# Optimization experiments

Hardware: AMD Instinct MI355X
Metric: run time of the kernel (lower is better)

## Reference

```python
import jax, jax.numpy as jnp
import numpy as np

B, H, D = 512, 2048, 4096          # batch, mem_hid_dim, r_dim + r2_dim
MAXITER = 100
LR = 0.01                          # mem_step_size
TOL = 1e-6
B1, B2, EPS = 0.9, 0.999, 1e-8     # torch.optim.Adam defaults


def setup_inputs() -> dict:
    key = jax.random.key(0)
    k = jax.random.split(key, 5)
    x = jax.random.normal(k[0], (B, D), jnp.float32)
    W = jax.random.normal(k[1], (D, H), jnp.float32) * 0.02   # mem.weight (out, in)
    c = jax.random.normal(k[2], (D,), jnp.float32) * 0.01     # mem.bias
    b = jax.random.normal(k[3], (H,), jnp.float32) * 0.01     # prior mean self.b
    r0 = jax.random.normal(k[4], (B, H), jnp.float32) * 0.025 # init_code_
    return {"x": x, "W": W, "c": c, "b": b, "r0": r0}


def _infer(x, W, c, b, r0):
    batch = x.shape[0]

    def loss_and_grad(r):
        diff = x - (r @ W.T + c)                         # (B, D) residual
        pr = r - b                                       # (B, H) prior residual
        loss = (jnp.sum(diff * diff, axis=1) + jnp.sum(pr * pr, axis=1)).mean()
        # d loss / d r  (mean over batch, sum over features)
        grad = (2.0 / batch) * (pr - diff @ W)           # (B, H)
        return loss, grad

    def step(carry, _):
        r, m, v, t, done = carry
        loss, g = loss_and_grad(r)
        t1 = t + 1.0
        m1 = B1 * m + (1.0 - B1) * g
        v1 = B2 * v + (1.0 - B2) * g * g
        mhat = m1 / (1.0 - B1 ** t1)
        vhat = v1 / (1.0 - B2 ** t1)
        r1 = r - LR * mhat / (jnp.sqrt(vhat) + EPS)
        new_done = done | (jnp.linalg.norm(r1 - r) < TOL)
        sel = lambda new, old: jnp.where(done, old, new)  # freeze state after convergence
        return (sel(r1, r), sel(m1, m), sel(v1, v), sel(t1, t), new_done), loss

    init = (r0, jnp.zeros_like(r0), jnp.zeros_like(r0), jnp.float32(0.0), jnp.array(False))
    (r, _, _, _, _), losses = jax.lax.scan(step, init, None, length=MAXITER)
    return r, losses


def reference(x, W, c, b, r0):
    # Returns (inferred latent code r, per-iteration inference losses).
    return _infer(x, W, c, b, r0)
```

## Files before the change

kernel.cpp:

```cpp
#include <hip/hip_runtime.h>
#include <cmath>


#define B_SZ 512
#define H_SZ 2048
#define D_SZ 4096
#define ITERS 100

typedef __attribute__((ext_vector_type(8))) short short8;
typedef __attribute__((ext_vector_type(4))) float f32x4;

__device__ __forceinline__ unsigned short f2bf(float f) {
    unsigned u = __float_as_uint(f);
    u = (u + 0x7fffu + ((u >> 16) & 1u)) >> 16;
    return (unsigned short)u;
}
__device__ __forceinline__ float bflo(unsigned mv) { return __uint_as_float(mv << 16); }
__device__ __forceinline__ float bfhi(unsigned mv) { return __uint_as_float(mv & 0xffff0000u); }

__device__ __forceinline__ void gload_lds16(const unsigned short* g, unsigned short* l) {
    __builtin_amdgcn_global_load_lds((const __attribute__((address_space(1))) void*)g,
                                     (__attribute__((address_space(3))) void*)l, 16, 0, 0);
}

__global__ __launch_bounds__(256) void k_transpose(const float* __restrict__ W,
                                                   unsigned short* __restrict__ Wt) {
    __shared__ unsigned short tile[64][72];
    const int d0 = blockIdx.x * 64, h0 = blockIdx.y * 64;
    const int t = threadIdx.x;
    const int lr = t >> 6, lc = t & 63;
#pragma unroll
    for (int rr = 0; rr < 16; ++rr) {
        const int dl = rr * 4 + lr;
        tile[dl][lc] = f2bf(W[(size_t)(d0 + dl) * H_SZ + h0 + lc]);
    }
    __syncthreads();
#pragma unroll
    for (int rr = 0; rr < 16; ++rr) {
        const int hl = rr * 4 + lr;
        Wt[(size_t)(h0 + hl) * D_SZ + d0 + lc] = tile[lc][hl];
    }
}

__global__ __launch_bounds__(256) void k_prepx(const float* __restrict__ x, const float* __restrict__ c,
                                               unsigned short* __restrict__ xcbf, float* __restrict__ xc2) {
    const int b = blockIdx.x, t = threadIdx.x;
    const float* xr = x + (size_t)b * D_SZ;
    unsigned short* orow = xcbf + (size_t)b * D_SZ;
    float acc = 0.f;
#pragma unroll
    for (int ch = 0; ch < 2; ++ch) {
        const int base = (ch * 256 + t) * 8;
        const float4 v0 = *(const float4*)(xr + base);
        const float4 v1 = *(const float4*)(xr + base + 4);
        const float4 c0 = *(const float4*)(c + base);
        const float4 c1 = *(const float4*)(c + base + 4);
        const float e0 = v0.x - c0.x, e1 = v0.y - c0.y, e2 = v0.z - c0.z, e3 = v0.w - c0.w;
        const float e4 = v1.x - c1.x, e5 = v1.y - c1.y, e6 = v1.z - c1.z, e7 = v1.w - c1.w;
        acc += e0 * e0 + e1 * e1 + e2 * e2 + e3 * e3 + e4 * e4 + e5 * e5 + e6 * e6 + e7 * e7;
        short8 ov;
        ov[0] = (short)f2bf(e0); ov[1] = (short)f2bf(e1); ov[2] = (short)f2bf(e2); ov[3] = (short)f2bf(e3);
        ov[4] = (short)f2bf(e4); ov[5] = (short)f2bf(e5); ov[6] = (short)f2bf(e6); ov[7] = (short)f2bf(e7);
        *(short8*)(orow + base) = ov;
    }
#pragma unroll
    for (int off = 32; off > 0; off >>= 1) acc += __shfl_down(acc, off);
    __shared__ float wred[4];
    if ((t & 63) == 0) wred[t >> 6] = acc;
    __syncthreads();
    if (t == 0) xc2[b] = wred[0] + wred[1] + wred[2] + wred[3];
}

__global__ __launch_bounds__(256) void k_init(const float* __restrict__ r0, float* __restrict__ r,
                                              unsigned* __restrict__ mv,
                                              unsigned short* __restrict__ rbfA) {
    const size_t i = (size_t)blockIdx.x * 256 + threadIdx.x;
#pragma unroll
    for (int k = 0; k < 4; ++k) {
        const size_t idx = i + (size_t)k * 262144;
        const float val = r0[idx];
        r[idx] = val; mv[idx] = 0u; rbfA[idx] = f2bf(val);
    }
}

template <int TM, int EPI>
__global__ __launch_bounds__(256) void gemm64(
        const unsigned short* __restrict__ A, int lda,
        const unsigned short* __restrict__ Bt, int ldb, int K,
        unsigned short* __restrict__ Cb, float* __restrict__ Cf, int ldc) {
    __shared__ alignas(16) unsigned short Al[2][TM * 64];
    __shared__ alignas(16) unsigned short Bl[2][64 * 64];
    const int t = threadIdx.x, w = t >> 6, lane = t & 63;
    const int m0 = blockIdx.y * TM, n0 = blockIdx.x * 64;
    constexpr int NJ = (TM == 64) ? 2 : 1;
    const int row_base = (TM == 64) ? (w >> 1) * 32 : 0;
    const int col_base = (TM == 64) ? (w & 1) * 32 : w * 16;

    f32x4 acc[2][NJ] = {};

    auto stage = [&](int buf, int k0) {
#pragma unroll
        for (int h = 0; h < 2; ++h) {
            const int c = h * 256 + t;
            const int row = c >> 3, g = c & 7;
            const int gl = g ^ (row & 7);
            gload_lds16(Bt + (size_t)(n0 + row) * ldb + k0 + gl * 8, &Bl[buf][(h * 256 + w * 64) * 8]);
        }
        if constexpr (TM == 64) {
#pragma unroll
            for (int h = 0; h < 2; ++h) {
                const int c = h * 256 + t;
                const int row = c >> 3, g = c & 7;
                const int gl = g ^ (row & 7);
                gload_lds16(A + (size_t)(m0 + row) * lda + k0 + gl * 8, &Al[buf][(h * 256 + w * 64) * 8]);
            }
        } else {
            const int row = t >> 3, g = t & 7;
            const int gl = g ^ (row & 7);
            gload_lds16(A + (size_t)(m0 + row) * lda + k0 + gl * 8, &Al[buf][(w * 64) * 8]);
        }
    };

    stage(0, 0);
    const int nK = K >> 6;
    for (int kt = 0; kt < nK; ++kt) {
        __syncthreads();
        const int cur = kt & 1;
        if (kt + 1 < nK) stage(cur ^ 1, (kt + 1) << 6);
        const unsigned short* a_base = Al[cur];
        const unsigned short* b_base = Bl[cur];
#pragma unroll
        for (int kh = 0; kh < 2; ++kh) {
            short8 av[2], bv[NJ];
#pragma unroll
            for (int i = 0; i < 2; ++i) {
                const int row = row_base + i * 16 + (lane & 15);
                const int g = (kh * 4 + (lane >> 4)) ^ (row & 7);
                av[i] = *(const short8*)(a_base + row * 64 + g * 8);
            }
#pragma unroll
            for (int j = 0; j < NJ; ++j) {
                const int row = col_base + j * 16 + (lane & 15);
                const int g = (kh * 4 + (lane >> 4)) ^ (row & 7);
                bv[j] = *(const short8*)(b_base + row * 64 + g * 8);
            }
#pragma unroll
            for (int i = 0; i < 2; ++i)
#pragma unroll
                for (int j = 0; j < NJ; ++j)
                    acc[i][j] = __builtin_amdgcn_mfma_f32_16x16x32_bf16(av[i], bv[j], acc[i][j], 0, 0, 0);
        }
    }

#pragma unroll
    for (int i = 0; i < 2; ++i)
#pragma unroll
        for (int j = 0; j < NJ; ++j) {
            const int col = n0 + col_base + j * 16 + (lane & 15);
            const int row0 = m0 + row_base + i * 16 + ((lane >> 4) << 2);
#pragma unroll
            for (int q = 0; q < 4; ++q) {
                if constexpr (EPI == 0) Cb[(size_t)(row0 + q) * ldc + col] = f2bf(acc[i][j][q]);
                else Cf[(size_t)(row0 + q) * ldc + col] = acc[i][j][q];
            }
        }
}

__global__ __launch_bounds__(1024) void gemm_q(
        const unsigned short* __restrict__ Ain,
        const unsigned short* __restrict__ G,
        const float* __restrict__ rin,
        float* __restrict__ rout,
        unsigned* __restrict__ mv,
        const float* __restrict__ ubuf,
        const float* __restrict__ bvec,
        unsigned short* __restrict__ rbf_out,
        float* __restrict__ lossPart,
        float inv1, float inv2) {
    __shared__ alignas(16) unsigned short stg[8][2][64 * 64];
    __shared__ float wred[16];
    const int t = threadIdx.x, w = t >> 6, lane = t & 63;
    const int bid = blockIdx.x;
    const int m0 = (bid >> 5) * 64;
    const int n0 = ((bid & 7) * 4 + ((bid >> 3) & 3)) * 64;
    const int qd = w & 3, gr = w >> 2;
    const int qrow = (qd >> 1) * 32, qcol = (qd & 1) * 32;
    const int rlo = lane & 15, hi = lane >> 4;

    const int col0 = n0 + qcol + (gr & 1) * 16 + rlo;
    const int rowb = m0 + qrow + (gr >> 1) * 16 + (hi << 2);
    float pre_r[4], pre_u[4];
    unsigned pre_mv[4];
    const float pre_b = bvec[col0];
#pragma unroll
    for (int q = 0; q < 4; ++q) {
        const size_t idx = (size_t)(rowb + q) * H_SZ + col0;
        pre_r[q] = rin[idx]; pre_u[q] = ubuf[idx]; pre_mv[q] = mv[idx];
    }
    __builtin_amdgcn_sched_barrier(0);

    const int tt = t & 255;
    auto stage = [&](int buf, int s) {
        const int kbase = gr * 512 + s * 64;
#pragma unroll
        for (int c = 0; c < 2; ++c) {
            const int idx = c * 256 + tt;
            const int row = idx >> 3, g = idx & 7;
            const int gl = g ^ (row & 7);
            gload_lds16(Ain + (size_t)(m0 + row) * H_SZ + kbase + gl * 8, &stg[gr][buf][idx * 8]);
            gload_lds16(G + (size_t)(n0 + row) * H_SZ + kbase + gl * 8, &stg[4 + gr][buf][idx * 8]);
        }
    };

    stage(0, 0);
    f32x4 acc[2][2] = {};
    for (int s = 0; s < 8; ++s) {
        __syncthreads();
        const int cur = s & 1;
        if (s + 1 < 8) stage(cur ^ 1, s + 1);
        const unsigned short* a_base = stg[gr][cur];
        const unsigned short* b_base = stg[4 + gr][cur];
#pragma unroll
        for (int kh = 0; kh < 2; ++kh) {
            short8 av[2], bv[2];
#pragma unroll
            for (int i = 0; i < 2; ++i) {
                const int row = qrow + i * 16 + rlo;
                av[i] = *(const short8*)(a_base + row * 64 + ((kh * 4 + hi) ^ (row & 7)) * 8);
            }
#pragma unroll
            for (int j = 0; j < 2; ++j) {
                const int row = qcol + j * 16 + rlo;
                bv[j] = *(const short8*)(b_base + row * 64 + ((kh * 4 + hi) ^ (row & 7)) * 8);
            }
#pragma unroll
            for (int i = 0; i < 2; ++i)
#pragma unroll
                for (int j = 0; j < 2; ++j)
                    acc[i][j] = __builtin_amdgcn_mfma_f32_16x16x32_bf16(av[i], bv[j], acc[i][j], 0, 0, 0);
        }
    }

    __syncthreads();
    float* scr = (float*)stg;
    const int wbase = (w * 64 + lane) * 17;
#pragma unroll
    for (int i = 0; i < 2; ++i)
#pragma unroll
        for (int j = 0; j < 2; ++j)
#pragma unroll
            for (int q = 0; q < 4; ++q)
                scr[wbase + (i * 2 + j) * 4 + q] = acc[i][j][q];
    __syncthreads();

    float sval[4];
#pragma unroll
    for (int q = 0; q < 4; ++q) {
        float s = 0.f;
#pragma unroll
        for (int g = 0; g < 4; ++g)
            s += scr[((g * 4 + qd) * 64 + lane) * 17 + gr * 4 + q];
        sval[q] = s;
    }

    float lpart = 0.f;
#pragma unroll
    for (int q = 0; q < 4; ++q) {
        const size_t idx = (size_t)(rowb + q) * H_SZ + col0;
        const float s = sval[q];
        const float rold = pre_r[q];
        const float ue = pre_u[q];
        const float g = (2.0f / B_SZ) * (rold - pre_b - ue + s);
        lpart += (rold - pre_b) * (rold - pre_b) + rold * (s - 2.0f * ue);
        const float m1 = 0.9f * bflo(pre_mv[q]) + 0.1f * g;
        const float v1 = 0.999f * bfhi(pre_mv[q]) + 0.001f * (g * g);
        mv[idx] = (unsigned)f2bf(m1) | ((unsigned)f2bf(v1) << 16);
        const float rn = rold - 0.01f * (m1 * inv1) / (sqrtf(v1 * inv2) + 1e-8f);
        rout[idx] = rn;
        if (rbf_out) rbf_out[idx] = f2bf(rn);
    }
#pragma unroll
    for (int off = 32; off > 0; off >>= 1) lpart += __shfl_down(lpart, off);
    if (lane == 0) wred[w] = lpart;
    __syncthreads();
    if (t == 0) {
        float sum = 0.f;
#pragma unroll
        for (int k = 0; k < 16; ++k) sum += wred[k];
        lossPart[bid] = sum;
    }
}

__global__ __launch_bounds__(256) void k_finalize(const float* __restrict__ lossPart,
                                                  const float* __restrict__ xc2, float* __restrict__ out) {
    const int it = blockIdx.x, t = threadIdx.x;
    float p = lossPart[it * 256 + t] + xc2[t] + xc2[t + 256];
#pragma unroll
    for (int off = 32; off > 0; off >>= 1) p += __shfl_down(p, off);
    __shared__ float wred[4];
    if ((t & 63) == 0) wred[t >> 6] = p;
    __syncthreads();
    if (t == 0) out[(size_t)B_SZ * H_SZ + it] = (wred[0] + wred[1] + wred[2] + wred[3]) * (1.0f / B_SZ);
}

extern "C" void kernel_launch(void* const* d_in, const int* in_sizes, int n_in,
                              void* d_out, int out_size, void* d_ws, size_t ws_size,
                              hipStream_t stream) {
    const float* x = (const float*)d_in[0];
    const float* W = (const float*)d_in[1];
    const float* cvec = (const float*)d_in[2];
    const float* bvec = (const float*)d_in[3];
    const float* r0 = (const float*)d_in[4];
    float* out = (float*)d_out;
    char* ws = (char*)d_ws;

    unsigned short* Wt = (unsigned short*)(ws);
    unsigned short* Gbf = (unsigned short*)(ws + 16777216);
    unsigned short* xcbf = (unsigned short*)(ws + 25165824);
    float* u = (float*)(ws + 29360128);
    float* r = (float*)(ws + 33554432);
    unsigned* mv = (unsigned*)(ws + 37748736);
    unsigned short* rbfA = (unsigned short*)(ws + 41943040);
    unsigned short* rbfB = (unsigned short*)(ws + 44040192);
    float* xc2 = (float*)(ws + 46137344);
    float* lossPart = (float*)(ws + 46139392);

    k_transpose<<<dim3(64, 32), 256, 0, stream>>>(W, Wt);
    k_prepx<<<512, 256, 0, stream>>>(x, cvec, xcbf, xc2);
    k_init<<<1024, 256, 0, stream>>>(r0, r, mv, rbfA);
    gemm64<64, 0><<<dim3(32, 32), 256, 0, stream>>>(Wt, D_SZ, Wt, D_SZ, D_SZ, Gbf, nullptr, H_SZ);
    gemm64<32, 1><<<dim3(32, 16), 256, 0, stream>>>(xcbf, D_SZ, Wt, D_SZ, D_SZ, nullptr, u, H_SZ);

    for (int it = 0; it < ITERS; ++it) {
        const float inv1 = (float)(1.0 / (1.0 - std::pow(0.9, (double)(it + 1))));
        const float inv2 = (float)(1.0 / (1.0 - std::pow(0.999, (double)(it + 1))));
        const unsigned short* rin_bf = (it & 1) ? rbfB : rbfA;
        unsigned short* rout_bf = (it + 1 < ITERS) ? ((it & 1) ? rbfA : rbfB) : nullptr;
        float* rout_f = (it + 1 < ITERS) ? r : out;
        gemm_q<<<256, 1024, 0, stream>>>(rin_bf, Gbf, r, rout_f, mv, u, bvec, rout_bf,
                                         lossPart + (size_t)it * 256, inv1, inv2);
    }
    k_finalize<<<ITERS, 256, 0, stream>>>(lossPart, xc2, out);
}
```

Before: 1.576 ms.

## Triple-buffer A tiles and prefetch two stages ahead with manual waitcnt

```diff
diff --git a/kernel.cpp b/kernel.cpp
--- a/kernel.cpp
+++ b/kernel.cpp
@@ -177,8 +177,8 @@
         unsigned short* __restrict__ rbf_out,
         float* __restrict__ lossPart,
         float inv1, float inv2) {
-    __shared__ alignas(16) unsigned short stg[8][2][64 * 64];
-    __shared__ float wred[16];
+    __shared__ alignas(16) unsigned short Ab[3][4][4096];
+    __shared__ alignas(16) unsigned short Bb[2][4][4096];
     const int t = threadIdx.x, w = t >> 6, lane = t & 63;
     const int bid = blockIdx.x;
     const int m0 = (bid >> 5) * 64;
@@ -200,26 +200,39 @@
     __builtin_amdgcn_sched_barrier(0);
 
     const int tt = t & 255;
-    auto stage = [&](int buf, int s) {
+    auto stageA = [&](int buf, int s) {
         const int kbase = gr * 512 + s * 64;
 #pragma unroll
         for (int c = 0; c < 2; ++c) {
             const int idx = c * 256 + tt;
             const int row = idx >> 3, g = idx & 7;
             const int gl = g ^ (row & 7);
-            gload_lds16(Ain + (size_t)(m0 + row) * H_SZ + kbase + gl * 8, &stg[gr][buf][idx * 8]);
-            gload_lds16(G + (size_t)(n0 + row) * H_SZ + kbase + gl * 8, &stg[4 + gr][buf][idx * 8]);
+            gload_lds16(Ain + (size_t)(m0 + row) * H_SZ + kbase + gl * 8, &Ab[buf][gr][idx * 8]);
         }
     };
-
-    stage(0, 0);
+    auto stageB = [&](int buf, int s) {
+        const int kbase = gr * 512 + s * 64;
+#pragma unroll
+        for (int c = 0; c < 2; ++c) {
+            const int idx = c * 256 + tt;
+            const int row = idx >> 3, g = idx & 7;
+            const int gl = g ^ (row & 7);
+            gload_lds16(G + (size_t)(n0 + row) * H_SZ + kbase + gl * 8, &Bb[buf][gr][idx * 8]);
+        }
+    };
+
+    stageA(0, 0); stageB(0, 0); stageA(1, 1);
+
     f32x4 acc[2][2] = {};
     for (int s = 0; s < 8; ++s) {
-        __syncthreads();
-        const int cur = s & 1;
-        if (s + 1 < 8) stage(cur ^ 1, s + 1);
-        const unsigned short* a_base = stg[gr][cur];
-        const unsigned short* b_base = stg[4 + gr][cur];
+        if (s < 7) asm volatile("s_waitcnt vmcnt(2) lgkmcnt(0)" ::: "memory");
+        else       asm volatile("s_waitcnt vmcnt(0) lgkmcnt(0)" ::: "memory");
+        __builtin_amdgcn_s_barrier();
+        __builtin_amdgcn_sched_barrier(0);
+        if (s + 1 < 8) stageB((s + 1) & 1, s + 1);
+        if (s + 2 < 8) stageA((s + 2) % 3, s + 2);
+        const unsigned short* a_base = Ab[s % 3][gr];
+        const unsigned short* b_base = Bb[s & 1][gr];
 #pragma unroll
         for (int kh = 0; kh < 2; ++kh) {
             short8 av[2], bv[2];
@@ -242,7 +255,8 @@
     }
 
     __syncthreads();
-    float* scr = (float*)stg;
+    float* scr = (float*)Ab;
+    float* wred = scr + 20000;
     const int wbase = (w * 64 + lane) * 17;
 #pragma unroll
     for (int i = 0; i < 2; ++i)
```

After: 1.429 ms (median of 2 runs). 1.1x faster.
